# Optimization experiments

Hardware: AMD Instinct MI355X
Metric: run time of the kernel (lower is better)

## Reference

```python
import jax, jax.numpy as jnp
import numpy as np

N = 100000   # nodes
E = 1600000  # edges (avg degree 16)
D = 128      # in = hid = out dim
EPS = 1e-5   # BatchNorm eps


def setup_inputs() -> dict:
    key = jax.random.key(0)
    ks = jax.random.split(key, 14)
    x = jax.random.normal(ks[0], (N, D), dtype=jnp.float32)
    row = jax.random.randint(ks[1], (E,), 0, N, dtype=jnp.int32)
    col = jax.random.randint(ks[2], (E,), 0, N, dtype=jnp.int32)
    edge_weight = jax.random.uniform(ks[3], (E,), dtype=jnp.float32)
    s = 1.0 / np.sqrt(D)
    W0 = jax.random.uniform(ks[4], (D, D), jnp.float32, -s, s)
    b0 = jax.random.uniform(ks[5], (D,), jnp.float32, -s, s)
    W1 = jax.random.uniform(ks[6], (D, D), jnp.float32, -s, s)
    b1 = jax.random.uniform(ks[7], (D,), jnp.float32, -s, s)
    W2 = jax.random.uniform(ks[8], (D, D), jnp.float32, -s, s)
    b2 = jax.random.uniform(ks[9], (D,), jnp.float32, -s, s)
    g0 = jnp.ones((D,), jnp.float32); be0 = jnp.zeros((D,), jnp.float32)
    g1 = jnp.ones((D,), jnp.float32); be1 = jnp.zeros((D,), jnp.float32)
    return {"x": x, "edge_weight": edge_weight,
            "W0": W0, "b0": b0, "g0": g0, "be0": be0,
            "W1": W1, "b1": b1, "g1": g1, "be1": be1,
            "W2": W2, "b2": b2, "row": row, "col": col}


def _spmm(edge_weight, row, col, h):
    # (A_norm @ h) with A in COO: out[r] = sum_e w_e * h[col_e] for row_e == r
    return jax.ops.segment_sum(edge_weight[:, None] * h[col], row, num_segments=N)


def _bn(h, gamma, beta):
    # BatchNorm1d, training-mode stats (biased variance), over the node axis
    m = h.mean(axis=0)
    v = h.var(axis=0)
    return gamma * (h - m) * jax.lax.rsqrt(v + EPS) + beta


def reference(x, edge_weight, W0, b0, g0, be0, W1, b1, g1, be1, W2, b2, row, col):
    # hidden block 1: SpMM(A, Linear(h)) -> BN -> ReLU (dropout p=0)
    h = jax.nn.relu(_bn(_spmm(edge_weight, row, col, x @ W0 + b0), g0, be0))
    # hidden block 2
    h = jax.nn.relu(_bn(_spmm(edge_weight, row, col, h @ W1 + b1), g1, be1))
    # final layer: SpMM(A, Linear(h)), no BN/activation
    return _spmm(edge_weight, row, col, h @ W2 + b2)
```

## Files before the change

### kernel.cpp

```cpp
#include <hip/hip_runtime.h>
#include <cstddef>

#define DD 128
#define EPS 1e-5f

typedef short short8 __attribute__((ext_vector_type(8)));
typedef float float4v __attribute__((ext_vector_type(4)));

__device__ __forceinline__ unsigned short f2bf(float f) {
    union { float f; unsigned int u; } x; x.f = f;
    unsigned int r = x.u + 0x7fffu + ((x.u >> 16) & 1u);
    return (unsigned short)(r >> 16);
}
__device__ __forceinline__ float bfhi2f(unsigned int hi_bits) {
    union { unsigned int u; float f; } x; x.u = hi_bits;
    return x.f;
}


__global__ void hist_kernel(const int* __restrict__ row, int* __restrict__ deg, int E) {
    int e = blockIdx.x * blockDim.x + threadIdx.x;
    if (e < E) atomicAdd(&deg[row[e]], 1);
}

__global__ void scanA_kernel(const int* __restrict__ deg, int* __restrict__ tmp,
                             int* __restrict__ bsum, int n) {
    __shared__ int s[1024];
    int tid = threadIdx.x;
    int gid = blockIdx.x * 1024 + tid;
    int v = (gid < n) ? deg[gid] : 0;
    s[tid] = v;
    __syncthreads();
    for (int off = 1; off < 1024; off <<= 1) {
        int t = s[tid];
        int u = (tid >= off) ? s[tid - off] : 0;
        __syncthreads();
        s[tid] = t + u;
        __syncthreads();
    }
    if (gid < n) tmp[gid] = s[tid];
    if (tid == 1023) bsum[blockIdx.x] = s[1023];
}

__global__ void scanB_kernel(const int* __restrict__ bsum, int* __restrict__ boff,
                             int* __restrict__ row_start, int nb, int n) {
    __shared__ int s[128];
    int tid = threadIdx.x;
    int v = (tid < nb) ? bsum[tid] : 0;
    s[tid] = v;
    __syncthreads();
    for (int off = 1; off < 128; off <<= 1) {
        int t = s[tid];
        int u = (tid >= off) ? s[tid - off] : 0;
        __syncthreads();
        s[tid] = t + u;
        __syncthreads();
    }
    if (tid < nb) boff[tid] = s[tid] - v;
    if (tid == nb - 1) row_start[n] = s[tid];
}

__global__ void scanC_kernel(const int* __restrict__ deg, const int* __restrict__ tmp,
                             const int* __restrict__ boff, int* __restrict__ row_start,
                             int* __restrict__ cursor, int* __restrict__ bcur, int n) {
    int gid = blockIdx.x * 1024 + threadIdx.x;
    if (gid < n) {
        int rs = tmp[gid] - deg[gid] + boff[blockIdx.x];
        row_start[gid] = rs;
        cursor[gid] = rs;
        if ((gid & 255) == 0) bcur[gid >> 8] = rs;
    }
}


__global__ __launch_bounds__(256) void scatter_phase1_kernel(
    const int* __restrict__ row, const int* __restrict__ col,
    const float* __restrict__ ew, int* __restrict__ bcur,
    unsigned long long* __restrict__ ebuf2, int E, int nbuck) {
    __shared__ int hist[512];
    __shared__ int cur[512];
    int tid = threadIdx.x;
    int b = blockIdx.x;
    int C = (E + gridDim.x - 1) / gridDim.x;
    int e0 = b * C, e1 = min(E, e0 + C);
    for (int t = tid; t < nbuck; t += 256) hist[t] = 0;
    __syncthreads();
    for (int e = e0 + tid; e < e1; e += 256)
        atomicAdd(&hist[row[e] >> 8], 1);
    __syncthreads();
    for (int i = tid; i < nbuck; i += 256) {
        int t = i + b * 37;
        t -= (t >= nbuck) ? nbuck * (t / nbuck) : 0;
        int h = hist[t];
        cur[t] = h ? atomicAdd(&bcur[t], h) : 0;
    }
    __syncthreads();
    for (int e = e0 + tid; e < e1; e += 256) {
        int r = row[e];
        int bk = r >> 8;
        int pos = atomicAdd(&cur[bk], 1);
        unsigned long long pk = (unsigned long long)((unsigned int)col[e]
                              | ((unsigned int)(r & 255) << 24))
                              | ((unsigned long long)__float_as_uint(ew[e]) << 32);
        ebuf2[pos] = pk;
    }
}

#define P2CAP 6144

__global__ __launch_bounds__(256) void scatter_phase2_kernel(
    const unsigned long long* __restrict__ ebuf2, const int* __restrict__ row_start,
    int* __restrict__ cursor, unsigned long long* __restrict__ ebuf, int N) {
    __shared__ int cur[256];
    __shared__ unsigned long long outb[P2CAP];
    int b = blockIdx.x;
    int r_lo = b << 8;
    int r_hi = min(N, r_lo + 256);
    int e_lo = row_start[r_lo];
    int e_hi = row_start[r_hi];
    int cnt = e_hi - e_lo;
    int tid = threadIdx.x;
    if (cnt <= P2CAP) {
        int r = r_lo + tid;
        cur[tid] = (r < N) ? (row_start[r] - e_lo) : 0;
        __syncthreads();
        for (int i = e_lo + tid; i < e_hi; i += 256) {
            unsigned long long pk = ebuf2[i];
            int rl = (int)((unsigned int)(pk >> 24) & 255u);
            int pos = atomicAdd(&cur[rl], 1);
            outb[pos] = pk & 0xFFFFFFFF0001FFFFull;
        }
        __syncthreads();
        for (int i = tid; i < cnt; i += 256)
            ebuf[e_lo + i] = outb[i];
    } else {
        for (int i = e_lo + tid; i < e_hi; i += 256) {
            unsigned long long pk = ebuf2[i];
            int rl = (int)((unsigned int)(pk >> 24) & 255u);
            int pos = atomicAdd(&cursor[r_lo + rl], 1);
            ebuf[pos] = pk & 0xFFFFFFFF0001FFFFull;
        }
    }
}


__global__ void convw_kernel(const float* __restrict__ W0, const float* __restrict__ W1,
                             const float* __restrict__ W2, unsigned short* __restrict__ T0,
                             unsigned short* __restrict__ T1, unsigned short* __restrict__ T2) {
    const float* W = (blockIdx.y == 0) ? W0 : (blockIdx.y == 1) ? W1 : W2;
    unsigned short* T = (blockIdx.y == 0) ? T0 : (blockIdx.y == 1) ? T1 : T2;
    int gid = blockIdx.x * 256 + threadIdx.x;
    int k = gid >> 7, n = gid & 127;
    T[n * DD + k] = f2bf(W[k * DD + n]);
}


__global__ __launch_bounds__(256) void gemm_mfma_f32_kernel(
    const float* __restrict__ A, const unsigned short* __restrict__ Wt,
    const float* __restrict__ bias, unsigned short* __restrict__ H, int nrows)
{
    __shared__ unsigned short Asl[64][136];
    __shared__ unsigned short Wsl[128][136];

    const int tid  = threadIdx.x;
    const int row0 = blockIdx.x * 64;

    for (int i = tid; i < 2048; i += 256) {
        int r = i >> 4, off = (i & 15) * 8;
        *(uint4*)&Wsl[r][off] = *(const uint4*)(Wt + (size_t)r * DD + off);
    }
    __syncthreads();

    const int w = tid >> 6, lane = tid & 63;
    const int m = lane & 15, q = lane >> 4;
    const int grow = row0 + w * 16 + m;
    const bool inb = grow < nrows;

    short8 afr[4];
    #pragma unroll
    for (int c = 0; c < 4; ++c) {
        float4 v0 = make_float4(0.f, 0.f, 0.f, 0.f);
        float4 v1 = v0;
        if (inb) {
            v0 = *(const float4*)(A + (size_t)grow * DD + c * 32 + q * 8);
            v1 = *(const float4*)(A + (size_t)grow * DD + c * 32 + q * 8 + 4);
        }
        short8 t;
        t[0] = (short)f2bf(v0.x); t[1] = (short)f2bf(v0.y);
        t[2] = (short)f2bf(v0.z); t[3] = (short)f2bf(v0.w);
        t[4] = (short)f2bf(v1.x); t[5] = (short)f2bf(v1.y);
        t[6] = (short)f2bf(v1.z); t[7] = (short)f2bf(v1.w);
        afr[c] = t;
    }

    float4v acc[8];
    #pragma unroll
    for (int t = 0; t < 8; ++t) acc[t] = (float4v){0.f, 0.f, 0.f, 0.f};

    #pragma unroll
    for (int t = 0; t < 8; ++t) {
        #pragma unroll
        for (int c = 0; c < 4; ++c) {
            short8 bfr = *(const short8*)&Wsl[t * 16 + m][c * 32 + q * 8];
            acc[t] = __builtin_amdgcn_mfma_f32_16x16x32_bf16(afr[c], bfr, acc[t], 0, 0, 0);
        }
    }

    #pragma unroll
    for (int t = 0; t < 8; ++t) {
        float bv = bias[t * 16 + m];
        #pragma unroll
        for (int i = 0; i < 4; ++i)
            Asl[w * 16 + q * 4 + i][t * 16 + m] = f2bf(acc[t][i] + bv);
    }
    __syncthreads();

    for (int i = tid; i < 1024; i += 256) {
        int r = i >> 4, off = (i & 15) * 8;
        if (row0 + r < nrows)
            *(uint4*)(H + (size_t)(row0 + r) * DD + off) = *(const uint4*)&Asl[r][off];
    }
}


__global__ __launch_bounds__(256) void gemm_mfma_bf16_kernel(
    const unsigned int* __restrict__ A, const unsigned short* __restrict__ Wt,
    const float* __restrict__ bias,
    const float* __restrict__ sums, const float* __restrict__ g,
    const float* __restrict__ be,
    unsigned short* __restrict__ H, int nrows)
{
    __shared__ unsigned short Asl[64][136];
    __shared__ unsigned short Wsl[128][136];
    __shared__ float scl_s[128], sft_s[128];

    const int tid  = threadIdx.x;
    const int row0 = blockIdx.x * 64;

    if (tid < 128) {
        float inv_n = 1.0f / (float)nrows;
        float mean = sums[tid] * inv_n;
        float var = sums[128 + tid] * inv_n - mean * mean;
        float rstd = rsqrtf(var + EPS);
        float sc = g[tid] * rstd;
        scl_s[tid] = sc;
        sft_s[tid] = be[tid] - mean * sc;
    }

    for (int i = tid; i < 2048; i += 256) {
        int r = i >> 4, off = (i & 15) * 8;
        *(uint4*)&Wsl[r][off] = *(const uint4*)(Wt + (size_t)r * DD + off);
    }
    __syncthreads();

    const int w = tid >> 6, lane = tid & 63;
    const int m = lane & 15, q = lane >> 4;
    const int grow = row0 + w * 16 + m;
    const bool inb = grow < nrows;

    short8 afr[4];
    #pragma unroll
    for (int c = 0; c < 4; ++c) {
        uint4 ua = make_uint4(0, 0, 0, 0);
        if (inb)
            ua = *(const uint4*)(A + (size_t)grow * 64 + c * 16 + q * 4);
        unsigned int uu[4] = {ua.x, ua.y, ua.z, ua.w};
        short8 t;
        #pragma unroll
        for (int j = 0; j < 4; ++j) {
            int k = c * 32 + q * 8 + 2 * j;
            float vx = fmaxf(0.f, bfhi2f(uu[j] << 16) * scl_s[k] + sft_s[k]);
            float vy = fmaxf(0.f, bfhi2f(uu[j] & 0xffff0000u) * scl_s[k + 1] + sft_s[k + 1]);
            t[2 * j]     = (short)f2bf(vx);
            t[2 * j + 1] = (short)f2bf(vy);
        }
        afr[c] = t;
    }

    float4v acc[8];
    #pragma unroll
    for (int t = 0; t < 8; ++t) acc[t] = (float4v){0.f, 0.f, 0.f, 0.f};

    #pragma unroll
    for (int t = 0; t < 8; ++t) {
        #pragma unroll
        for (int c = 0; c < 4; ++c) {
            short8 bfr = *(const short8*)&Wsl[t * 16 + m][c * 32 + q * 8];
            acc[t] = __builtin_amdgcn_mfma_f32_16x16x32_bf16(afr[c], bfr, acc[t], 0, 0, 0);
        }
    }

    #pragma unroll
    for (int t = 0; t < 8; ++t) {
        float bv = bias[t * 16 + m];
        #pragma unroll
        for (int i = 0; i < 4; ++i)
            Asl[w * 16 + q * 4 + i][t * 16 + m] = f2bf(acc[t][i] + bv);
    }
    __syncthreads();

    for (int i = tid; i < 1024; i += 256) {
        int r = i >> 4, off = (i & 15) * 8;
        if (row0 + r < nrows)
            *(uint4*)(H + (size_t)(row0 + r) * DD + off) = *(const uint4*)&Asl[r][off];
    }
}


__global__ __launch_bounds__(256, 8) void spmm_bf16_kernel(
    const unsigned short* __restrict__ H, const int* __restrict__ row_start,
    const unsigned long long* __restrict__ ebuf,
    float* __restrict__ Sf, unsigned int* __restrict__ Sb, int writeBF, int N, int K)
{
    const int lane = threadIdx.x & 63;
    const int g = lane >> 4;
    const int p = lane & 15;
    const int wave = (blockIdx.x << 2) | (threadIdx.x >> 6);
    int r0 = wave * K;
    if (r0 >= N) return;
    int r1 = min(N, r0 + K);

    const unsigned short* Hp = H + p * 8;
    const unsigned long long* Ep = ebuf + g;

    for (int r = r0; r < r1; ++r) {
        int e = row_start[r];
        const int e1 = row_start[r + 1];
        float acc[8];
        #pragma unroll
        for (int j = 0; j < 8; ++j) acc[j] = 0.f;

        for (; e + 15 < e1; e += 16) {
            unsigned long long pk[4];
            #pragma unroll
            for (int j = 0; j < 4; ++j)
                pk[j] = __builtin_nontemporal_load(Ep + e + j * 4);
            uint4 u[4];
            #pragma unroll
            for (int j = 0; j < 4; ++j)
                u[j] = *(const uint4*)(Hp + (size_t)(unsigned int)pk[j] * DD);
            #pragma unroll
            for (int j = 0; j < 4; ++j) {
                float wj = __uint_as_float((unsigned int)(pk[j] >> 32));
                unsigned int uu[4] = {u[j].x, u[j].y, u[j].z, u[j].w};
                #pragma unroll
                for (int q = 0; q < 4; ++q) {
                    acc[2 * q]     += wj * bfhi2f(uu[q] << 16);
                    acc[2 * q + 1] += wj * bfhi2f(uu[q] & 0xffff0000u);
                }
            }
        }
        for (; e + 7 < e1; e += 8) {
            unsigned long long pk[2];
            #pragma unroll
            for (int j = 0; j < 2; ++j)
                pk[j] = __builtin_nontemporal_load(Ep + e + j * 4);
            uint4 u[2];
            #pragma unroll
            for (int j = 0; j < 2; ++j)
                u[j] = *(const uint4*)(Hp + (size_t)(unsigned int)pk[j] * DD);
            #pragma unroll
            for (int j = 0; j < 2; ++j) {
                float wj = __uint_as_float((unsigned int)(pk[j] >> 32));
                unsigned int uu[4] = {u[j].x, u[j].y, u[j].z, u[j].w};
                #pragma unroll
                for (int q = 0; q < 4; ++q) {
                    acc[2 * q]     += wj * bfhi2f(uu[q] << 16);
                    acc[2 * q + 1] += wj * bfhi2f(uu[q] & 0xffff0000u);
                }
            }
        }
        if (e + 3 < e1) {
            unsigned long long pk = __builtin_nontemporal_load(Ep + e);
            uint4 u = *(const uint4*)(Hp + (size_t)(unsigned int)pk * DD);
            float wj = __uint_as_float((unsigned int)(pk >> 32));
            unsigned int uu[4] = {u.x, u.y, u.z, u.w};
            #pragma unroll
            for (int q = 0; q < 4; ++q) {
                acc[2 * q]     += wj * bfhi2f(uu[q] << 16);
                acc[2 * q + 1] += wj * bfhi2f(uu[q] & 0xffff0000u);
            }
            e += 4;
        }
        if (e < e1) {
            int idx = e + g;
            unsigned long long pk = (idx < e1) ? __builtin_nontemporal_load(&ebuf[idx]) : 0ull;
            uint4 u = *(const uint4*)(Hp + (size_t)(unsigned int)pk * DD);
            float wj = __uint_as_float((unsigned int)(pk >> 32));
            unsigned int uu[4] = {u.x, u.y, u.z, u.w};
            #pragma unroll
            for (int q = 0; q < 4; ++q) {
                acc[2 * q]     += wj * bfhi2f(uu[q] << 16);
                acc[2 * q + 1] += wj * bfhi2f(uu[q] & 0xffff0000u);
            }
        }

        #pragma unroll
        for (int j = 0; j < 8; ++j) {
            acc[j] += __shfl_xor(acc[j], 16);
            acc[j] += __shfl_xor(acc[j], 32);
        }

        if (g == 0) {
            if (writeBF) {
                unsigned int o[4];
                #pragma unroll
                for (int j = 0; j < 4; ++j)
                    o[j] = (unsigned int)f2bf(acc[2 * j])
                         | ((unsigned int)f2bf(acc[2 * j + 1]) << 16);
                *(uint4*)(Sb + (size_t)r * 64 + p * 4) = *(const uint4*)o;
            } else {
                float4 lo = make_float4(acc[0], acc[1], acc[2], acc[3]);
                float4 hi = make_float4(acc[4], acc[5], acc[6], acc[7]);
                *(float4*)(Sf + (size_t)r * DD + p * 8) = lo;
                *(float4*)(Sf + (size_t)r * DD + p * 8 + 4) = hi;
            }
        }
    }
}


__global__ void bn_stats_bf16_kernel(const unsigned int* __restrict__ Sb,
                                     float* __restrict__ sums, int n) {
    __shared__ float lsx[256], lsx2[256], lsy[256], lsy2[256];
    int tid = threadIdx.x;
    int c2 = tid & 63;
    float sx = 0.f, sx2 = 0.f, sy = 0.f, sy2 = 0.f;
    int total = n * 64;
    for (int i = blockIdx.x * 256 + tid; i < total; i += 256 * 256) {
        unsigned int u = Sb[i];
        float vx = bfhi2f(u << 16);
        float vy = bfhi2f(u & 0xffff0000u);
        sx += vx; sx2 += vx * vx;
        sy += vy; sy2 += vy * vy;
    }
    lsx[tid] = sx; lsx2[tid] = sx2; lsy[tid] = sy; lsy2[tid] = sy2;
    __syncthreads();
    if (tid < 64) {
        sx  = lsx[tid]  + lsx[tid + 64]  + lsx[tid + 128]  + lsx[tid + 192];
        sx2 = lsx2[tid] + lsx2[tid + 64] + lsx2[tid + 128] + lsx2[tid + 192];
        sy  = lsy[tid]  + lsy[tid + 64]  + lsy[tid + 128]  + lsy[tid + 192];
        sy2 = lsy2[tid] + lsy2[tid + 64] + lsy2[tid + 128] + lsy2[tid + 192];
        atomicAdd(&sums[2 * c2], sx);
        atomicAdd(&sums[2 * c2 + 1], sy);
        atomicAdd(&sums[128 + 2 * c2], sx2);
        atomicAdd(&sums[129 + 2 * c2], sy2);
    }
}


extern "C" void kernel_launch(void* const* d_in, const int* in_sizes, int n_in,
                              void* d_out, int out_size, void* d_ws, size_t ws_size,
                              hipStream_t stream) {
    const float* x   = (const float*)d_in[0];
    const float* ew  = (const float*)d_in[1];
    const float* W0  = (const float*)d_in[2];
    const float* b0  = (const float*)d_in[3];
    const float* g0  = (const float*)d_in[4];
    const float* be0 = (const float*)d_in[5];
    const float* W1  = (const float*)d_in[6];
    const float* b1  = (const float*)d_in[7];
    const float* g1  = (const float*)d_in[8];
    const float* be1 = (const float*)d_in[9];
    const float* W2  = (const float*)d_in[10];
    const float* b2  = (const float*)d_in[11];
    const int* row   = (const int*)d_in[12];
    const int* col   = (const int*)d_in[13];

    const int N = in_sizes[0] / DD;
    const int E = in_sizes[1];
    float* out = (float*)d_out;

    char* w = (char*)d_ws;
    unsigned short* H   = (unsigned short*)w; w += (size_t)N * DD * 2;
    unsigned int* Sb    = (unsigned int*)w;   w += (size_t)N * 64 * 4;
    unsigned long long* ebuf = (unsigned long long*)w; w += (size_t)E * 8;
    unsigned short* Wt0 = (unsigned short*)w; w += DD * DD * 2;
    unsigned short* Wt1 = (unsigned short*)w; w += DD * DD * 2;
    unsigned short* Wt2 = (unsigned short*)w; w += DD * DD * 2;
    float* sums         = (float*)w;          w += 256 * 4;
    int*   deg          = (int*)w;            w += (size_t)N * 4;
    int*   tmp          = (int*)w;            w += (size_t)N * 4;
    int*   cursor       = (int*)w;            w += (size_t)N * 4;
    int*   bsum         = (int*)w;            w += 128 * 4;
    int*   boff         = (int*)w;            w += 128 * 4;
    int*   row_start    = (int*)w;            w += (size_t)(N + 1) * 4;

    unsigned long long* ebuf2 = (unsigned long long*)Sb;
    int* bcur = tmp;
    int nbuck = (N + 255) >> 8;

    hipMemsetAsync(deg, 0, (size_t)N * 4, stream);
    hist_kernel<<<(E + 255) / 256, 256, 0, stream>>>(row, deg, E);
    int NB = (N + 1023) / 1024;
    scanA_kernel<<<NB, 1024, 0, stream>>>(deg, tmp, bsum, N);
    scanB_kernel<<<1, 128, 0, stream>>>(bsum, boff, row_start, NB, N);
    scanC_kernel<<<NB, 1024, 0, stream>>>(deg, tmp, boff, row_start, cursor, bcur, N);
    scatter_phase1_kernel<<<256, 256, 0, stream>>>(row, col, ew, bcur, ebuf2, E, nbuck);
    scatter_phase2_kernel<<<nbuck, 256, 0, stream>>>(ebuf2, row_start, cursor, ebuf, N);

    convw_kernel<<<dim3(64, 3), 256, 0, stream>>>(W0, W1, W2, Wt0, Wt1, Wt2);

    int gblocks = (N + 63) / 64;

    const int SPMM_BLOCKS = 2048;
    const int totalWaves = SPMM_BLOCKS * 4;
    const int K = (N + totalWaves - 1) / totalWaves;

    gemm_mfma_f32_kernel<<<gblocks, 256, 0, stream>>>(x, Wt0, b0, H, N);
    spmm_bf16_kernel<<<SPMM_BLOCKS, 256, 0, stream>>>(H, row_start, ebuf, nullptr, Sb, 1, N, K);
    hipMemsetAsync(sums, 0, 256 * 4, stream);
    bn_stats_bf16_kernel<<<256, 256, 0, stream>>>(Sb, sums, N);

    gemm_mfma_bf16_kernel<<<gblocks, 256, 0, stream>>>(Sb, Wt1, b1, sums, g0, be0, H, N);
    spmm_bf16_kernel<<<SPMM_BLOCKS, 256, 0, stream>>>(H, row_start, ebuf, nullptr, Sb, 1, N, K);
    hipMemsetAsync(sums, 0, 256 * 4, stream);
    bn_stats_bf16_kernel<<<256, 256, 0, stream>>>(Sb, sums, N);

    gemm_mfma_bf16_kernel<<<gblocks, 256, 0, stream>>>(Sb, Wt2, b2, sums, g1, be1, H, N);
    spmm_bf16_kernel<<<SPMM_BLOCKS, 256, 0, stream>>>(H, row_start, ebuf, out, nullptr, 0, N, K);
}
```

Baseline: 567.2 us.

## Make CSR scatter and BN statistics deterministic with explicit scans instead of atomics

The bucket scatter's first phase no longer reserves bucket offsets with global atomics. It now writes a per-block histogram matrix, scans it per bucket in a separate kernel, and then writes edges using the precomputed offsets. The BN statistics kernel writes per-block partial sums, and a single-block kernel reduces them, which replaces the float atomics and the memset. Together these remove atomic contention and make the results deterministic, at the cost of extra kernel launches and an extra read of the row array.

After: 581.4 us. 1.02x slower.

```diff
diff --git a/kernel.cpp b/kernel.cpp
--- a/kernel.cpp
+++ b/kernel.cpp
@@ -62,23 +62,19 @@
 
 __global__ void scanC_kernel(const int* __restrict__ deg, const int* __restrict__ tmp,
                              const int* __restrict__ boff, int* __restrict__ row_start,
-                             int* __restrict__ cursor, int* __restrict__ bcur, int n) {
+                             int* __restrict__ cursor, int n) {
     int gid = blockIdx.x * 1024 + threadIdx.x;
     if (gid < n) {
         int rs = tmp[gid] - deg[gid] + boff[blockIdx.x];
         row_start[gid] = rs;
         cursor[gid] = rs;
-        if ((gid & 255) == 0) bcur[gid >> 8] = rs;
-    }
-}
-
-
-__global__ __launch_bounds__(256) void scatter_phase1_kernel(
-    const int* __restrict__ row, const int* __restrict__ col,
-    const float* __restrict__ ew, int* __restrict__ bcur,
-    unsigned long long* __restrict__ ebuf2, int E, int nbuck) {
+    }
+}
+
+
+__global__ __launch_bounds__(256) void scatter_hist_kernel(
+    const int* __restrict__ row, int* __restrict__ hmat, int E, int nbuck) {
     __shared__ int hist[512];
-    __shared__ int cur[512];
     int tid = threadIdx.x;
     int b = blockIdx.x;
     int C = (E + gridDim.x - 1) / gridDim.x;
@@ -88,12 +84,39 @@
     for (int e = e0 + tid; e < e1; e += 256)
         atomicAdd(&hist[row[e] >> 8], 1);
     __syncthreads();
-    for (int i = tid; i < nbuck; i += 256) {
-        int t = i + b * 37;
-        t -= (t >= nbuck) ? nbuck * (t / nbuck) : 0;
-        int h = hist[t];
-        cur[t] = h ? atomicAdd(&bcur[t], h) : 0;
-    }
+    for (int t = tid; t < nbuck; t += 256)
+        hmat[t * 256 + b] = hist[t];
+}
+
+__global__ __launch_bounds__(256) void scatter_scan_kernel(
+    const int* __restrict__ hmat, const int* __restrict__ row_start,
+    int* __restrict__ omat) {
+    __shared__ int s[256];
+    int t = blockIdx.x;
+    int tid = threadIdx.x;
+    int v = hmat[t * 256 + tid];
+    s[tid] = v;
+    __syncthreads();
+    for (int off = 1; off < 256; off <<= 1) {
+        int a = s[tid];
+        int u = (tid >= off) ? s[tid - off] : 0;
+        __syncthreads();
+        s[tid] = a + u;
+        __syncthreads();
+    }
+    omat[t * 256 + tid] = row_start[t << 8] + s[tid] - v;
+}
+
+__global__ __launch_bounds__(256) void scatter_write_kernel(
+    const int* __restrict__ row, const int* __restrict__ col,
+    const float* __restrict__ ew, const int* __restrict__ omat,
+    unsigned long long* __restrict__ ebuf2, int E, int nbuck) {
+    __shared__ int cur[512];
+    int tid = threadIdx.x;
+    int b = blockIdx.x;
+    int C = (E + gridDim.x - 1) / gridDim.x;
+    int e0 = b * C, e1 = min(E, e0 + C);
+    for (int t = tid; t < nbuck; t += 256) cur[t] = omat[t * 256 + b];
     __syncthreads();
     for (int e = e0 + tid; e < e1; e += 256) {
         int r = row[e];
@@ -421,7 +444,7 @@
 
 
 __global__ void bn_stats_bf16_kernel(const unsigned int* __restrict__ Sb,
-                                     float* __restrict__ sums, int n) {
+                                     float* __restrict__ pbuf, int n) {
     __shared__ float lsx[256], lsx2[256], lsy[256], lsy2[256];
     int tid = threadIdx.x;
     int c2 = tid & 63;
@@ -441,11 +464,25 @@
         sx2 = lsx2[tid] + lsx2[tid + 64] + lsx2[tid + 128] + lsx2[tid + 192];
         sy  = lsy[tid]  + lsy[tid + 64]  + lsy[tid + 128]  + lsy[tid + 192];
         sy2 = lsy2[tid] + lsy2[tid + 64] + lsy2[tid + 128] + lsy2[tid + 192];
-        atomicAdd(&sums[2 * c2], sx);
-        atomicAdd(&sums[2 * c2 + 1], sy);
-        atomicAdd(&sums[128 + 2 * c2], sx2);
-        atomicAdd(&sums[129 + 2 * c2], sy2);
-    }
+        float* pb = pbuf + (size_t)blockIdx.x * 256;
+        pb[2 * c2]       = sx;
+        pb[2 * c2 + 1]   = sy;
+        pb[128 + 2 * c2] = sx2;
+        pb[129 + 2 * c2] = sy2;
+    }
+}
+
+__global__ __launch_bounds__(1024) void bn_final_kernel(
+    const float* __restrict__ pbuf, float* __restrict__ sums, int nb) {
+    __shared__ float red[1024];
+    int c = threadIdx.x & 255, j = threadIdx.x >> 8;
+    float s = 0.f;
+    for (int b = j; b < nb; b += 4)
+        s += pbuf[(size_t)b * 256 + c];
+    red[threadIdx.x] = s;
+    __syncthreads();
+    if (threadIdx.x < 256)
+        sums[c] = red[c] + red[c + 256] + red[c + 512] + red[c + 768];
 }
 
 
@@ -479,6 +516,9 @@
     unsigned short* Wt1 = (unsigned short*)w; w += DD * DD * 2;
     unsigned short* Wt2 = (unsigned short*)w; w += DD * DD * 2;
     float* sums         = (float*)w;          w += 256 * 4;
+    float* pbuf         = (float*)w;          w += 256 * 256 * 4;
+    int*   hmat         = (int*)w;            w += 512 * 256 * 4;
+    int*   omat         = (int*)w;            w += 512 * 256 * 4;
     int*   deg          = (int*)w;            w += (size_t)N * 4;
     int*   tmp          = (int*)w;            w += (size_t)N * 4;
     int*   cursor       = (int*)w;            w += (size_t)N * 4;
@@ -487,7 +527,6 @@
     int*   row_start    = (int*)w;            w += (size_t)(N + 1) * 4;
 
     unsigned long long* ebuf2 = (unsigned long long*)Sb;
-    int* bcur = tmp;
     int nbuck = (N + 255) >> 8;
 
     hipMemsetAsync(deg, 0, (size_t)N * 4, stream);
@@ -495,8 +534,10 @@
     int NB = (N + 1023) / 1024;
     scanA_kernel<<<NB, 1024, 0, stream>>>(deg, tmp, bsum, N);
     scanB_kernel<<<1, 128, 0, stream>>>(bsum, boff, row_start, NB, N);
-    scanC_kernel<<<NB, 1024, 0, stream>>>(deg, tmp, boff, row_start, cursor, bcur, N);
-    scatter_phase1_kernel<<<256, 256, 0, stream>>>(row, col, ew, bcur, ebuf2, E, nbuck);
+    scanC_kernel<<<NB, 1024, 0, stream>>>(deg, tmp, boff, row_start, cursor, N);
+    scatter_hist_kernel<<<256, 256, 0, stream>>>(row, hmat, E, nbuck);
+    scatter_scan_kernel<<<nbuck, 256, 0, stream>>>(hmat, row_start, omat);
+    scatter_write_kernel<<<256, 256, 0, stream>>>(row, col, ew, omat, ebuf2, E, nbuck);
     scatter_phase2_kernel<<<nbuck, 256, 0, stream>>>(ebuf2, row_start, cursor, ebuf, N);
 
     convw_kernel<<<dim3(64, 3), 256, 0, stream>>>(W0, W1, W2, Wt0, Wt1, Wt2);
@@ -509,13 +550,13 @@
 
     gemm_mfma_f32_kernel<<<gblocks, 256, 0, stream>>>(x, Wt0, b0, H, N);
     spmm_bf16_kernel<<<SPMM_BLOCKS, 256, 0, stream>>>(H, row_start, ebuf, nullptr, Sb, 1, N, K);
-    hipMemsetAsync(sums, 0, 256 * 4, stream);
-    bn_stats_bf16_kernel<<<256, 256, 0, stream>>>(Sb, sums, N);
+    bn_stats_bf16_kernel<<<256, 256, 0, stream>>>(Sb, pbuf, N);
+    bn_final_kernel<<<1, 1024, 0, stream>>>(pbuf, sums, 256);
 
     gemm_mfma_bf16_kernel<<<gblocks, 256, 0, stream>>>(Sb, Wt1, b1, sums, g0, be0, H, N);
     spmm_bf16_kernel<<<SPMM_BLOCKS, 256, 0, stream>>>(H, row_start, ebuf, nullptr, Sb, 1, N, K);
-    hipMemsetAsync(sums, 0, 256 * 4, stream);
-    bn_stats_bf16_kernel<<<256, 256, 0, stream>>>(Sb, sums, N);
+    bn_stats_bf16_kernel<<<256, 256, 0, stream>>>(Sb, pbuf, N);
+    bn_final_kernel<<<1, 1024, 0, stream>>>(pbuf, sums, 256);
 
     gemm_mfma_bf16_kernel<<<gblocks, 256, 0, stream>>>(Sb, Wt2, b2, sums, g1, be1, H, N);
     spmm_bf16_kernel<<<SPMM_BLOCKS, 256, 0, stream>>>(H, row_start, ebuf, out, nullptr, 0, N, K);
```

## Merge CSR build into cooperative kernel and fold small launches into neighbors

Applied to the files above, without the earlier changes.

Replaces the memset, histogram and three scan kernels with one cooperative kernel that uses grid syncs, and keeps the old path as a fallback if the cooperative launch fails. The weight-transpose kernel is folded into extra blocks of scatter_phase1, and the BN-sum memsets are replaced by zeroing inside the preceding SpMM kernel. The goal is to cut kernel-launch and memset overhead. In exchange, the histogram now runs on only about 98 blocks of 1024 threads, and the grid syncs add their own cost.

Measured after the change: 726.5 us. 1.28x slower.

```diff
diff --git a/kernel.cpp b/kernel.cpp
--- a/kernel.cpp
+++ b/kernel.cpp
@@ -1,5 +1,8 @@
 #include <hip/hip_runtime.h>
+#include <hip/hip_cooperative_groups.h>
 #include <cstddef>
+
+namespace cg = cooperative_groups;
 
 #define DD 128
 #define EPS 1e-5f
@@ -15,6 +18,67 @@
 __device__ __forceinline__ float bfhi2f(unsigned int hi_bits) {
     union { unsigned int u; float f; } x; x.u = hi_bits;
     return x.f;
+}
+
+
+__global__ __launch_bounds__(1024) void csr_coop_kernel(
+    const int* __restrict__ row, int* __restrict__ deg, int* __restrict__ tmp,
+    int* __restrict__ bsum, int* __restrict__ boff, int* __restrict__ row_start,
+    int* __restrict__ cursor, int* __restrict__ bcur, int E, int n, int nb)
+{
+    cg::grid_group grid = cg::this_grid();
+    __shared__ int s[1024];
+    int tid = threadIdx.x;
+    int gid = blockIdx.x * 1024 + tid;
+    int nthreads = gridDim.x * 1024;
+
+    if (gid < n) deg[gid] = 0;
+    __threadfence();
+    grid.sync();
+
+    for (int e = gid; e < E; e += nthreads)
+        atomicAdd(&deg[row[e]], 1);
+    __threadfence();
+    grid.sync();
+
+    int v = (gid < n) ? deg[gid] : 0;
+    s[tid] = v;
+    __syncthreads();
+    for (int off = 1; off < 1024; off <<= 1) {
+        int t = s[tid];
+        int u = (tid >= off) ? s[tid - off] : 0;
+        __syncthreads();
+        s[tid] = t + u;
+        __syncthreads();
+    }
+    if (gid < n) tmp[gid] = s[tid];
+    if (tid == 1023) bsum[blockIdx.x] = s[1023];
+    __threadfence();
+    grid.sync();
+
+    if (blockIdx.x == 0) {
+        int vv = (tid < nb) ? bsum[tid] : 0;
+        s[tid] = vv;
+        __syncthreads();
+        for (int off = 1; off < 128; off <<= 1) {
+            int t = s[tid];
+            int u = (tid >= off && tid < 128) ? s[tid - off] : 0;
+            __syncthreads();
+            if (tid < 128) s[tid] = t + u;
+            __syncthreads();
+        }
+        if (tid < nb) boff[tid] = s[tid] - vv;
+        if (tid == nb - 1) row_start[n] = s[tid];
+    }
+    __threadfence();
+    grid.sync();
+
+    if (gid < n) {
+        int rs = tmp[gid] - deg[gid] + boff[blockIdx.x];
+        row_start[gid] = rs;
+        cursor[gid] = rs;
+        if ((gid & 255) == 0) bcur[gid >> 8] = rs;
+    }
 }
 
 
@@ -76,12 +140,25 @@
 __global__ __launch_bounds__(256) void scatter_phase1_kernel(
     const int* __restrict__ row, const int* __restrict__ col,
     const float* __restrict__ ew, int* __restrict__ bcur,
-    unsigned long long* __restrict__ ebuf2, int E, int nbuck) {
+    unsigned long long* __restrict__ ebuf2, int E, int nbuck,
+    const float* __restrict__ W0, const float* __restrict__ W1,
+    const float* __restrict__ W2, unsigned short* __restrict__ T0,
+    unsigned short* __restrict__ T1, unsigned short* __restrict__ T2) {
     __shared__ int hist[512];
     __shared__ int cur[512];
     int tid = threadIdx.x;
     int b = blockIdx.x;
-    int C = (E + gridDim.x - 1) / gridDim.x;
+    if (b >= 256) {
+        int gid = (b - 256) * 256 + tid;
+        int mi = gid >> 14;
+        int ei = gid & 16383;
+        const float* W = (mi == 0) ? W0 : (mi == 1) ? W1 : W2;
+        unsigned short* T = (mi == 0) ? T0 : (mi == 1) ? T1 : T2;
+        int k = ei >> 7, n2 = ei & 127;
+        T[n2 * DD + k] = f2bf(W[k * DD + n2]);
+        return;
+    }
+    int C = (E + 255) / 256;
     int e0 = b * C, e1 = min(E, e0 + C);
     for (int t = tid; t < nbuck; t += 256) hist[t] = 0;
     __syncthreads();
@@ -144,17 +221,6 @@
 }
 
 
-__global__ void convw_kernel(const float* __restrict__ W0, const float* __restrict__ W1,
-                             const float* __restrict__ W2, unsigned short* __restrict__ T0,
-                             unsigned short* __restrict__ T1, unsigned short* __restrict__ T2) {
-    const float* W = (blockIdx.y == 0) ? W0 : (blockIdx.y == 1) ? W1 : W2;
-    unsigned short* T = (blockIdx.y == 0) ? T0 : (blockIdx.y == 1) ? T1 : T2;
-    int gid = blockIdx.x * 256 + threadIdx.x;
-    int k = gid >> 7, n = gid & 127;
-    T[n * DD + k] = f2bf(W[k * DD + n]);
-}
-
-
 __global__ __launch_bounds__(256) void gemm_mfma_f32_kernel(
     const float* __restrict__ A, const unsigned short* __restrict__ Wt,
     const float* __restrict__ bias, unsigned short* __restrict__ H, int nrows)
@@ -310,8 +376,11 @@
 __global__ __launch_bounds__(256, 8) void spmm_bf16_kernel(
     const unsigned short* __restrict__ H, const int* __restrict__ row_start,
     const unsigned long long* __restrict__ ebuf,
-    float* __restrict__ Sf, unsigned int* __restrict__ Sb, int writeBF, int N, int K)
+    float* __restrict__ Sf, unsigned int* __restrict__ Sb, int writeBF,
+    float* __restrict__ zsum, int N, int K)
 {
+    if (zsum != nullptr && blockIdx.x == 0) zsum[threadIdx.x] = 0.f;
+
     const int lane = threadIdx.x & 63;
     const int g = lane >> 4;
     const int p = lane & 15;
@@ -488,18 +557,34 @@
 
     unsigned long long* ebuf2 = (unsigned long long*)Sb;
     int* bcur = tmp;
+    bcur = boff + 128;
+    bcur = (int*)w; w += 512 * 4;
+
     int nbuck = (N + 255) >> 8;
-
-    hipMemsetAsync(deg, 0, (size_t)N * 4, stream);
-    hist_kernel<<<(E + 255) / 256, 256, 0, stream>>>(row, deg, E);
     int NB = (N + 1023) / 1024;
-    scanA_kernel<<<NB, 1024, 0, stream>>>(deg, tmp, bsum, N);
-    scanB_kernel<<<1, 128, 0, stream>>>(bsum, boff, row_start, NB, N);
-    scanC_kernel<<<NB, 1024, 0, stream>>>(deg, tmp, boff, row_start, cursor, bcur, N);
-    scatter_phase1_kernel<<<256, 256, 0, stream>>>(row, col, ew, bcur, ebuf2, E, nbuck);
+
+    {
+        const int* row_a = row; int* deg_a = deg; int* tmp_a = tmp;
+        int* bsum_a = bsum; int* boff_a = boff; int* rs_a = row_start;
+        int* cur_a = cursor; int* bcur_a = bcur;
+        int E_a = E, N_a = N, NB_a = NB;
+        void* args[] = { &row_a, &deg_a, &tmp_a, &bsum_a, &boff_a, &rs_a,
+                         &cur_a, &bcur_a, &E_a, &N_a, &NB_a };
+        hipError_t ce = hipLaunchCooperativeKernel((const void*)csr_coop_kernel,
+                                                   dim3(NB), dim3(1024), args, 0, stream);
+        if (ce != hipSuccess) {
+            (void)hipGetLastError();
+            hipMemsetAsync(deg, 0, (size_t)N * 4, stream);
+            hist_kernel<<<(E + 255) / 256, 256, 0, stream>>>(row, deg, E);
+            scanA_kernel<<<NB, 1024, 0, stream>>>(deg, tmp, bsum, N);
+            scanB_kernel<<<1, 128, 0, stream>>>(bsum, boff, row_start, NB, N);
+            scanC_kernel<<<NB, 1024, 0, stream>>>(deg, tmp, boff, row_start, cursor, bcur, N);
+        }
+    }
+
+    scatter_phase1_kernel<<<448, 256, 0, stream>>>(row, col, ew, bcur, ebuf2, E, nbuck,
+                                                   W0, W1, W2, Wt0, Wt1, Wt2);
     scatter_phase2_kernel<<<nbuck, 256, 0, stream>>>(ebuf2, row_start, cursor, ebuf, N);
-
-    convw_kernel<<<dim3(64, 3), 256, 0, stream>>>(W0, W1, W2, Wt0, Wt1, Wt2);
 
     int gblocks = (N + 63) / 64;
 
@@ -508,15 +593,13 @@
     const int K = (N + totalWaves - 1) / totalWaves;
 
     gemm_mfma_f32_kernel<<<gblocks, 256, 0, stream>>>(x, Wt0, b0, H, N);
-    spmm_bf16_kernel<<<SPMM_BLOCKS, 256, 0, stream>>>(H, row_start, ebuf, nullptr, Sb, 1, N, K);
-    hipMemsetAsync(sums, 0, 256 * 4, stream);
+    spmm_bf16_kernel<<<SPMM_BLOCKS, 256, 0, stream>>>(H, row_start, ebuf, nullptr, Sb, 1, sums, N, K);
     bn_stats_bf16_kernel<<<256, 256, 0, stream>>>(Sb, sums, N);
 
     gemm_mfma_bf16_kernel<<<gblocks, 256, 0, stream>>>(Sb, Wt1, b1, sums, g0, be0, H, N);
-    spmm_bf16_kernel<<<SPMM_BLOCKS, 256, 0, stream>>>(H, row_start, ebuf, nullptr, Sb, 1, N, K);
-    hipMemsetAsync(sums, 0, 256 * 4, stream);
+    spmm_bf16_kernel<<<SPMM_BLOCKS, 256, 0, stream>>>(H, row_start, ebuf, nullptr, Sb, 1, sums, N, K);
     bn_stats_bf16_kernel<<<256, 256, 0, stream>>>(Sb, sums, N);
 
     gemm_mfma_bf16_kernel<<<gblocks, 256, 0, stream>>>(Sb, Wt2, b2, sums, g1, be1, H, N);
-    spmm_bf16_kernel<<<SPMM_BLOCKS, 256, 0, stream>>>(H, row_start, ebuf, out, nullptr, 0, N, K);
-}
+    spmm_bf16_kernel<<<SPMM_BLOCKS, 256, 0, stream>>>(H, row_start, ebuf, out, nullptr, 0, nullptr, N, K);
+}
```
